# Performance work log

Hardware: AMD Instinct MI355X
Metric: run time of the kernel (lower is better)

The kernel has to match this reference:

```python
import jax, jax.numpy as jnp
import numpy as np

V, K, E, H, B, T = 30000, 9, 300, 300, 64, 512


def _lstm_dir(pre, W_hh, reverse):
    # pre: [T, B, 4H] = x @ W_ih.T + b_ih + b_hh, torch gate order (i, f, g, o)
    Bsz = pre.shape[1]
    Hh = W_hh.shape[1]
    h0 = jnp.zeros((Bsz, Hh), pre.dtype)
    c0 = jnp.zeros((Bsz, Hh), pre.dtype)

    def step(carry, p):
        h, c = carry
        gates = p + h @ W_hh.T
        i, f, g, o = jnp.split(gates, 4, axis=-1)
        i = jax.nn.sigmoid(i)
        f = jax.nn.sigmoid(f)
        o = jax.nn.sigmoid(o)
        g = jnp.tanh(g)
        c = f * c + i * g
        h = o * jnp.tanh(c)
        return (h, c), h

    _, hs = jax.lax.scan(step, (h0, c0), pre, reverse=reverse)
    return hs  # [T, B, H], time-aligned with input (reverse dir handled by scan)


def _crf_loglik(em, tags, mask, start, end, trans):
    # torchcrf CRF log-likelihood, reduction='sum'. em: [B,T,K], mask: [B,T] float.
    em_sc = jnp.take_along_axis(em, tags[..., None], axis=-1)[..., 0]  # [B,T]
    tr_sc = trans[tags[:, :-1], tags[:, 1:]]                            # [B,T-1]
    seq_len = jnp.sum(mask, axis=1).astype(jnp.int32)                   # [B]
    last_tags = jnp.take_along_axis(tags, (seq_len - 1)[:, None], axis=1)[:, 0]
    num = start[tags[:, 0]] + em_sc[:, 0]
    num = num + jnp.sum((tr_sc + em_sc[:, 1:]) * mask[:, 1:], axis=1)
    num = num + end[last_tags]

    # forward algorithm (partition function)
    alpha0 = start[None, :] + em[:, 0]             # [B,K]
    em_t = jnp.swapaxes(em[:, 1:], 0, 1)           # [T-1,B,K]
    m_t = jnp.swapaxes(mask[:, 1:], 0, 1)          # [T-1,B]

    def step(alpha, xs):
        e, m = xs
        nxt = jax.nn.logsumexp(alpha[:, :, None] + trans[None] + e[:, None, :], axis=1)
        return jnp.where(m[:, None] > 0, nxt, alpha), None

    alpha, _ = jax.lax.scan(step, alpha0, (em_t, m_t))
    den = jax.nn.logsumexp(alpha + end[None, :], axis=1)
    return jnp.sum(num - den)


def _forward(x, y, embedding, W_ih_f, W_hh_f, b_ih_f, b_hh_f,
             W_ih_b, W_hh_b, b_ih_b, b_hh_b, W_lin, b_lin,
             start_trans, end_trans, trans):
    emb = embedding[x]                       # [B,T,E]
    emb_t = jnp.swapaxes(emb, 0, 1)          # [T,B,E]
    pre_f = emb_t @ W_ih_f.T + (b_ih_f + b_hh_f)
    pre_b = emb_t @ W_ih_b.T + (b_ih_b + b_hh_b)
    hs_f = _lstm_dir(pre_f, W_hh_f, reverse=False)
    hs_b = _lstm_dir(pre_b, W_hh_b, reverse=True)
    out = jnp.concatenate([hs_f, hs_b], axis=-1)  # [T,B,2H]
    out = jnp.swapaxes(out, 0, 1)                 # [B,T,2H]
    logits = out @ W_lin.T + b_lin
    probs = jax.nn.softmax(logits, axis=-1)
    mask = (y != -1).astype(probs.dtype)
    llh = _crf_loglik(probs, y, mask, start_trans, end_trans, trans)
    return probs, -llh


def setup_inputs() -> dict:
    key = jax.random.key(0)
    ks = jax.random.split(key, 17)

    def p(k, shape, s=0.05):
        return jax.random.normal(k, shape, dtype=jnp.float32) * s

    return {
        "x": jax.random.randint(ks[0], (B, T), 0, V),
        "y": jax.random.randint(ks[1], (B, T), 0, K),
        "embedding": p(ks[2], (V, E), 1.0),
        "W_ih_f": p(ks[3], (4 * H, E)),
        "W_hh_f": p(ks[4], (4 * H, H)),
        "b_ih_f": p(ks[5], (4 * H,)),
        "b_hh_f": p(ks[6], (4 * H,)),
        "W_ih_b": p(ks[7], (4 * H, E)),
        "W_hh_b": p(ks[8], (4 * H, H)),
        "b_ih_b": p(ks[9], (4 * H,)),
        "b_hh_b": p(ks[10], (4 * H,)),
        "W_lin": p(ks[11], (K, 2 * H)),
        "b_lin": p(ks[12], (K,)),
        "start_trans": p(ks[13], (K,), 0.1),
        "end_trans": p(ks[14], (K,), 0.1),
        "trans": p(ks[15], (K, K), 0.1),
    }


def reference(x, y, embedding, W_ih_f, W_hh_f, b_ih_f, b_hh_f,
              W_ih_b, W_hh_b, b_ih_b, b_hh_b, W_lin, b_lin,
              start_trans, end_trans, trans):
    return _forward(x, y, embedding, W_ih_f, W_hh_f, b_ih_f, b_hh_f,
                    W_ih_b, W_hh_b, b_ih_b, b_hh_b, W_lin, b_lin,
                    start_trans, end_trans, trans)
```

## Files before the change

kernel.cpp:

```cpp
#include <hip/hip_runtime.h>
#include <stdint.h>

#define TSEQ 512
#define NB   64
#define EMB  300
#define HID  300
#define G4   1200
#define KKP  150
#define NT   9
#define MTOT (TSEQ*NB)

#define NP 19
#define NQ 4
#define NWG (2*NQ*NP)
#define KSTEPS 10
#define HSTR 164
#define SENT64 0xFFFFFFFFFFFFFFFFull

typedef _Float16 f16x8 __attribute__((ext_vector_type(8)));
typedef float f32x4 __attribute__((ext_vector_type(4)));
union H2U { uint32_t u; _Float16 h[2]; };

__device__ __forceinline__ uint32_t packf2(float a, float b) {
  H2U u; u.h[0] = (_Float16)a; u.h[1] = (_Float16)b; return u.u;
}
__device__ __forceinline__ float fexp(float x) {
  return __builtin_amdgcn_exp2f(x * 1.44269504088896f);
}
__device__ __forceinline__ float sigm(float x) {
  return __builtin_amdgcn_rcpf(1.0f + fexp(-x));
}
__device__ __forceinline__ float ftanh(float x) {
  return 1.0f - 2.0f * __builtin_amdgcn_rcpf(fexp(2.0f * x) + 1.0f);
}

__global__ __launch_bounds__(256) void prep_wih(
    const float* __restrict__ Wihf, const float* __restrict__ Wihb,
    uint32_t* __restrict__ wtih) {
  int i = blockIdx.x * 256 + threadIdx.x;
  if (i >= KKP * G4) return;
  int m = blockIdx.y;
  int kk = i / G4, g = i % G4;
  const float* src = (m == 0) ? Wihf : Wihb;
  float2 v = *(const float2*)(src + (size_t)g * 300 + 2 * kk);
  wtih[(size_t)m * (KKP * G4) + i] = packf2(v.x, v.y);
}

__global__ __launch_bounds__(256) void prep_bias(
    const float* __restrict__ bihf, const float* __restrict__ bhhf,
    const float* __restrict__ bihb, const float* __restrict__ bhhb,
    float* __restrict__ bias) {
  int i = blockIdx.x * 256 + threadIdx.x;
  if (i < G4) {
    bias[i]       = bihf[i] + bhhf[i];
    bias[G4 + i]  = bihb[i] + bhhb[i];
  }
}

__global__ __launch_bounds__(64) void prep_w3(
    const float* __restrict__ Whhf, const float* __restrict__ Whhb,
    uint32_t* __restrict__ w2) {
  int blk = blockIdx.x;
  int ks = blk % KSTEPS; int tmp = blk / KSTEPS;
  int w = tmp & 3; tmp >>= 2;
  int p = tmp % NP; int d = tmp / NP;
  int lane = threadIdx.x;
  const float* W = d ? Whhb : Whhf;
  int m = lane & 15;
  int gamma = m >> 2, rr = m & 3;
  int hid = 16 * p + 4 * w + rr;
  int k0 = ks * 32 + (lane >> 4) * 8;
  float vals[8];
  #pragma unroll
  for (int e = 0; e < 8; ++e) {
    int k = k0 + e;
    vals[e] = (hid < 300 && k < 300) ? W[(size_t)(gamma * 300 + hid) * 300 + k] : 0.0f;
  }
  uint4 dw;
  dw.x = packf2(vals[0], vals[1]);
  dw.y = packf2(vals[2], vals[3]);
  dw.z = packf2(vals[4], vals[5]);
  dw.w = packf2(vals[6], vals[7]);
  *(uint4*)(w2 + ((size_t)blk * 64 + lane) * 4) = dw;
}

__global__ __launch_bounds__(256) void init_sent(uint32_t* __restrict__ ring) {
  size_t i = (size_t)blockIdx.x * 256 + threadIdx.x;
  if (i < 2457600ull)
    ((uint4*)ring)[i] = make_uint4(0xFFFFFFFFu, 0xFFFFFFFFu, 0xFFFFFFFFu, 0xFFFFFFFFu);
}

__global__ __launch_bounds__(256) void gather_emb(
    const int* __restrict__ x, const float* __restrict__ emb,
    uint32_t* __restrict__ Ae) {
  __shared__ __align__(16) uint32_t buf[64 * KKP];
  __shared__ int idxs[64];
  int tid = threadIdx.x;
  int m0 = blockIdx.x * 64;
  if (tid < 64) {
    int mm = m0 + tid;
    idxs[tid] = x[(size_t)(mm & 63) * TSEQ + (mm >> 6)];
  }
  __syncthreads();
  for (int i = tid; i < 64 * KKP; i += 256) {
    int mm = i / KKP, kk = i % KKP;
    float2 v = *(const float2*)(emb + (size_t)idxs[mm] * EMB + 2 * kk);
    buf[i] = packf2(v.x, v.y);
  }
  __syncthreads();
  for (int i = tid; i < 64 * KKP; i += 256) {
    int kk = i >> 6, mm = i & 63;
    Ae[(size_t)kk * MTOT + m0 + mm] = buf[mm * KKP + kk];
  }
}

__global__ __launch_bounds__(256) void embed_pre_mfma(
    const uint32_t* __restrict__ Ae, const uint32_t* __restrict__ wtih,
    const float* __restrict__ bias, _Float16* __restrict__ pre) {
  const int d = blockIdx.z;
  const int tid = threadIdx.x;
  const int w = tid >> 6, lane = tid & 63;
  const int n0 = blockIdx.x * 64 + w * 16;
  const int m00 = blockIdx.y * 128;
  const int col = n0 + (lane & 15);
  const bool colok = col < G4;
  const int rsel = lane >> 4;
  const uint32_t* Wd = wtih + (size_t)d * (KKP * G4);
  uint32_t bfr[KSTEPS][4];
  #pragma unroll
  for (int ks = 0; ks < KSTEPS; ++ks)
    #pragma unroll
    for (int j = 0; j < 4; ++j) {
      int kk = ks * 16 + rsel * 4 + j;
      bfr[ks][j] = (kk < KKP && colok) ? Wd[(size_t)kk * G4 + col] : 0u;
    }
  float bcol = colok ? bias[d * G4 + col] : 0.0f;
  for (int mb = 0; mb < 8; ++mb) {
    const int m0 = m00 + mb * 16;
    uint32_t afr[KSTEPS][4];
    #pragma unroll
    for (int ks = 0; ks < KSTEPS; ++ks)
      #pragma unroll
      for (int j = 0; j < 4; ++j) {
        int kk = ks * 16 + rsel * 4 + j;
        afr[ks][j] = (kk < KKP) ? Ae[(size_t)kk * MTOT + m0 + (lane & 15)] : 0u;
      }
    f32x4 acc; acc[0] = bcol; acc[1] = bcol; acc[2] = bcol; acc[3] = bcol;
    #pragma unroll
    for (int ks = 0; ks < KSTEPS; ++ks) {
      union { uint32_t u[4]; f16x8 v; } au, bu;
      au.u[0] = afr[ks][0]; au.u[1] = afr[ks][1]; au.u[2] = afr[ks][2]; au.u[3] = afr[ks][3];
      bu.u[0] = bfr[ks][0]; bu.u[1] = bfr[ks][1]; bu.u[2] = bfr[ks][2]; bu.u[3] = bfr[ks][3];
      acc = __builtin_amdgcn_mfma_f32_16x16x32_f16(au.v, bu.v, acc, 0, 0, 0);
    }
    if (colok) {
      #pragma unroll
      for (int j = 0; j < 4; ++j) {
        int m = m0 + rsel * 4 + j;
        pre[((size_t)d * MTOT + m) * G4 + col] = (_Float16)acc[j];
      }
    }
  }
}

__global__ __launch_bounds__(256, 1) void lstm_ring(
    const uint32_t* __restrict__ w2, const _Float16* __restrict__ pre,
    uint64_t* __restrict__ ring, uint32_t* __restrict__ hs16) {
  const int wg = blockIdx.x;
  const int p  = wg % NP;
  const int dq = wg / NP;
  const int q  = dq & 3;
  const int d  = dq >> 2;
  const int tid = threadIdx.x;
  const int w = tid >> 6, lane = tid & 63;
  const int G = lane >> 4, b = lane & 15;
  const int hidbase = 16 * p + 4 * w;
  const bool valid = hidbase < 300;
  const int bglob = 16 * q + b;

  __shared__ __align__(16) uint32_t hstg[2][16 * HSTR];
  __shared__ float xch[4][272];

  for (int i = tid; i < 2 * 16 * HSTR; i += 256) ((uint32_t*)hstg)[i] = 0u;

  uint4 afr[KSTEPS];
  const int blk0 = ((d * NP + p) * 4 + w) * KSTEPS;
  #pragma unroll
  for (int ks = 0; ks < KSTEPS; ++ks)
    afr[ks] = *(const uint4*)(w2 + ((size_t)(blk0 + ks) * 64 + lane) * 4);

  const int sb  = tid / 15;
  const int seg = tid % 15;
  const bool stg = tid < 240;

  float cstate = 0.0f;
  __syncthreads();

  for (int s = 0; s < TSEQ; ++s) {
    const int t = d ? (TSEQ - 1 - s) : s;
    const int cur = s & 1;

    uint2 pr = make_uint2(0u, 0u);
    if (valid)
      pr = *(const uint2*)(pre + ((size_t)d * MTOT + (size_t)t * NB + bglob) * G4
                           + (G * 300 + hidbase));

    if (s > 0 && stg) {
      const uint64_t* src = ring + ((size_t)(dq * TSEQ + (s - 1)) * 16 + sb) * 75 + seg * 5;
      uint64_t v[5];
      #pragma unroll
      for (int r = 0; r < 5; ++r)
        v[r] = __hip_atomic_load(src + r, __ATOMIC_RELAXED, __HIP_MEMORY_SCOPE_AGENT);
      uint32_t pend = 0x1Fu;
      while (pend) {
        #pragma unroll
        for (int r = 0; r < 5; ++r) {
          if (pend & (1u << r)) {
            if (v[r] != SENT64) pend &= ~(1u << r);
            else v[r] = __hip_atomic_load(src + r, __ATOMIC_RELAXED,
                                          __HIP_MEMORY_SCOPE_AGENT);
          }
        }
      }
      #pragma unroll
      for (int r = 0; r < 5; ++r)
        *(uint64_t*)&hstg[cur][sb * HSTR + 2 * (seg * 5 + r)] = v[r];
    }
    __syncthreads();

    f32x4 acc0, acc1;
    {
      H2U c0, c1; c0.u = pr.x; c1.u = pr.y;
      acc0[0] = (float)c0.h[0]; acc0[1] = (float)c0.h[1];
      acc0[2] = (float)c1.h[0]; acc0[3] = (float)c1.h[1];
      acc1[0] = 0.f; acc1[1] = 0.f; acc1[2] = 0.f; acc1[3] = 0.f;
    }
    #pragma unroll
    for (int ks = 0; ks < KSTEPS; ks += 2) {
      union { uint4 u; f16x8 v; } au0, au1, bu0, bu1;
      bu0.u = *(const uint4*)&hstg[cur][b * HSTR + ks * 16 + G * 4];
      bu1.u = *(const uint4*)&hstg[cur][b * HSTR + (ks + 1) * 16 + G * 4];
      au0.u = afr[ks]; au1.u = afr[ks + 1];
      acc0 = __builtin_amdgcn_mfma_f32_16x16x32_f16(au0.v, bu0.v, acc0, 0, 0, 0);
      acc1 = __builtin_amdgcn_mfma_f32_16x16x32_f16(au1.v, bu1.v, acc1, 0, 0, 0);
    }

    #pragma unroll
    for (int j = 0; j < 4; ++j)
      xch[w][(j * 4 + G) * 17 + b] = acc0[j] + acc1[j];
    asm volatile("s_waitcnt lgkmcnt(0)" ::: "memory");
    __builtin_amdgcn_sched_barrier(0);
    float gi = xch[w][(G * 4 + 0) * 17 + b];
    float gf = xch[w][(G * 4 + 1) * 17 + b];
    float gg = xch[w][(G * 4 + 2) * 17 + b];
    float go = xch[w][(G * 4 + 3) * 17 + b];

    float iv = sigm(gi), fv = sigm(gf), gv = ftanh(gg), ov = sigm(go);
    float c = fv * cstate + iv * gv; cstate = c;
    float h = ov * ftanh(c);

    float hp = __shfl_xor(h, 16);
    uint32_t dw = packf2(h, hp);
    uint32_t hi = __shfl_xor(dw, 32);
    if (valid && G == 0) {
      uint64_t val = (uint64_t)dw | ((uint64_t)hi << 32);
      __hip_atomic_store(
          ring + ((size_t)(dq * TSEQ + s) * 16 + b) * 75 + (4 * p + w),
          val, __ATOMIC_RELAXED, __HIP_MEMORY_SCOPE_AGENT);
      *(uint64_t*)(hs16 + ((size_t)d * MTOT + (size_t)t * NB + bglob) * 152
                   + (8 * p + 2 * w)) = val;
    }
  }
}

__global__ __launch_bounds__(256) void logits_probs(
    const uint32_t* __restrict__ hs16, const float* __restrict__ Wlin,
    const float* __restrict__ blin, float* __restrict__ probs) {
  __shared__ float Ws[NT * 600];
  __shared__ float bs[NT];
  int tid = threadIdx.x;
  for (int i = tid; i < NT * 600; i += 256) Ws[i] = Wlin[i];
  if (tid < NT) bs[tid] = blin[tid];
  __syncthreads();
  int wave = tid >> 6, lane = tid & 63;
  for (int it = 0; it < 4; ++it) {
    int tb = blockIdx.x * 16 + wave * 4 + it;
    const uint32_t* hf = hs16 + (size_t)tb * 152;
    const uint32_t* hb = hs16 + ((size_t)MTOT + tb) * 152;
    uint32_t fa[3], ga[3];
    fa[0] = hf[lane]; fa[1] = hf[64 + lane];
    fa[2] = (lane < 22) ? hf[128 + lane] : 0u;
    ga[0] = hb[lane]; ga[1] = hb[64 + lane];
    ga[2] = (lane < 22) ? hb[128 + lane] : 0u;
    float p[NT];
    #pragma unroll
    for (int k = 0; k < NT; ++k) p[k] = 0.f;
    #pragma unroll
    for (int c = 0; c < 3; ++c) {
      int kk = c * 64 + lane;
      if (kk < KKP) {
        H2U uf; uf.u = fa[c];
        H2U ug; ug.u = ga[c];
        float hf0 = (float)uf.h[0], hf1 = (float)uf.h[1];
        float hb0 = (float)ug.h[0], hb1 = (float)ug.h[1];
        #pragma unroll
        for (int k = 0; k < NT; ++k)
          p[k] += hf0 * Ws[k * 600 + 2 * kk] + hf1 * Ws[k * 600 + 2 * kk + 1]
                + hb0 * Ws[k * 600 + 300 + 2 * kk] + hb1 * Ws[k * 600 + 300 + 2 * kk + 1];
      }
    }
    #pragma unroll
    for (int off = 32; off > 0; off >>= 1)
      #pragma unroll
      for (int k = 0; k < NT; ++k) p[k] += __shfl_xor(p[k], off);
    float l[NT]; float mx = -1e30f;
    #pragma unroll
    for (int k = 0; k < NT; ++k) { l[k] = p[k] + bs[k]; mx = fmaxf(mx, l[k]); }
    float ssum = 0.f;
    #pragma unroll
    for (int k = 0; k < NT; ++k) ssum += expf(l[k] - mx);
    int t = tb >> 6, bb = tb & 63;
    if (lane < NT)
      probs[((size_t)bb * TSEQ + t) * NT + lane] = expf(l[lane] - mx) / ssum;
  }
}

__global__ __launch_bounds__(256) void crf_num(
    const int* __restrict__ y, const float* __restrict__ probs,
    const float* __restrict__ strt, const float* __restrict__ endt,
    const float* __restrict__ trans, float* __restrict__ nums) {
  int b = blockIdx.x, tid = threadIdx.x;
  __shared__ float r1[256], r2[256];
  float s = 0.f, cnt = 0.f;
  for (int t = tid; t < TSEQ; t += 256) {
    int yc = y[(size_t)b * TSEQ + t];
    cnt += (yc != -1) ? 1.f : 0.f;
    if (t >= 1) {
      int yp = y[(size_t)b * TSEQ + t - 1];
      float mask = (yc != -1) ? 1.f : 0.f;
      s += mask * (trans[yp * NT + yc] + probs[((size_t)b * TSEQ + t) * NT + yc]);
    }
  }
  r1[tid] = s; r2[tid] = cnt;
  __syncthreads();
  for (int off = 128; off > 0; off >>= 1) {
    if (tid < off) { r1[tid] += r1[tid + off]; r2[tid] += r2[tid + off]; }
    __syncthreads();
  }
  if (tid == 0) {
    int y0 = y[(size_t)b * TSEQ];
    int seqlen = (int)(r2[0] + 0.5f);
    int ylast = y[(size_t)b * TSEQ + seqlen - 1];
    nums[b] = strt[y0] + probs[((size_t)b * TSEQ) * NT + y0] + r1[0] + endt[ylast];
  }
}

__global__ __launch_bounds__(64) void crf_alpha(
    const int* __restrict__ y, const float* __restrict__ probs,
    const float* __restrict__ strt, const float* __restrict__ endt,
    const float* __restrict__ trans, float* __restrict__ dens) {
  int b = blockIdx.x, lane = threadIdx.x;
  __shared__ float P[TSEQ * NT];
  __shared__ float msk[TSEQ];
  for (int i = lane; i < TSEQ * NT; i += 64) P[i] = probs[(size_t)b * TSEQ * NT + i];
  for (int i = lane; i < TSEQ; i += 64) msk[i] = (y[(size_t)b * TSEQ + i] != -1) ? 1.f : 0.f;
  asm volatile("s_waitcnt lgkmcnt(0) vmcnt(0)" ::: "memory");
  int li = lane < NT ? lane : NT - 1;
  float trc[NT];
  #pragma unroll
  for (int j = 0; j < NT; ++j) trc[j] = trans[j * NT + li];
  float al = strt[li] + P[li];
  for (int t = 1; t < TSEQ; ++t) {
    float e = P[t * NT + li];
    float m = msk[t];
    float tmp[NT]; float mx = -1e30f;
    #pragma unroll
    for (int j = 0; j < NT; ++j) {
      float aj = __shfl(al, j);
      tmp[j] = aj + trc[j];
      mx = fmaxf(mx, tmp[j]);
    }
    float sum = 0.f;
    #pragma unroll
    for (int j = 0; j < NT; ++j) sum += expf(tmp[j] - mx);
    float nxt = e + mx + logf(sum);
    al = (m > 0.5f) ? nxt : al;
  }
  float vv = al + endt[li];
  float mx = -1e30f;
  #pragma unroll
  for (int j = 0; j < NT; ++j) mx = fmaxf(mx, __shfl(vv, j));
  float sum = 0.f;
  #pragma unroll
  for (int j = 0; j < NT; ++j) sum += expf(__shfl(vv, j) - mx);
  if (lane == 0) dens[b] = mx + logf(sum);
}

__global__ __launch_bounds__(64) void final_sum(
    const float* __restrict__ nums, const float* __restrict__ dens,
    float* __restrict__ out) {
  __shared__ float r[64];
  int tid = threadIdx.x;
  r[tid] = nums[tid] - dens[tid];
  __syncthreads();
  for (int off = 32; off > 0; off >>= 1) {
    if (tid < off) r[tid] += r[tid + off];
    __syncthreads();
  }
  if (tid == 0) out[(size_t)MTOT * NT] = -r[0];
}

extern "C" void kernel_launch(void* const* d_in, const int* in_sizes, int n_in,
                              void* d_out, int out_size, void* d_ws, size_t ws_size,
                              hipStream_t stream) {
  (void)in_sizes; (void)n_in; (void)out_size;
  const int*   x     = (const int*)d_in[0];
  const int*   y     = (const int*)d_in[1];
  const float* emb   = (const float*)d_in[2];
  const float* Wihf  = (const float*)d_in[3];
  const float* Whhf  = (const float*)d_in[4];
  const float* bihf  = (const float*)d_in[5];
  const float* bhhf  = (const float*)d_in[6];
  const float* Wihb  = (const float*)d_in[7];
  const float* Whhb  = (const float*)d_in[8];
  const float* bihb  = (const float*)d_in[9];
  const float* bhhb  = (const float*)d_in[10];
  const float* Wlin  = (const float*)d_in[11];
  const float* blin  = (const float*)d_in[12];
  const float* strt  = (const float*)d_in[13];
  const float* endt  = (const float*)d_in[14];
  const float* trans = (const float*)d_in[15];
  float* outp = (float*)d_out;

  char* ws = (char*)d_ws;
  const size_t OFF_WTIH = 0;
  const size_t OFF_W2   = 1440000;
  const size_t OFF_BIAS = 2996480;
  const size_t OFF_NUMS = 3006080;
  const size_t OFF_DENS = 3006336;
  const size_t OFF_RING = 3006592;
  const size_t OFF_HS16 = 42328192;
  const size_t OFF_PRE  = 82174080;
  if (ws_size < 239460480ull) return;

  uint32_t* wtih = (uint32_t*)(ws + OFF_WTIH);
  uint32_t* w2   = (uint32_t*)(ws + OFF_W2);
  float*    bias = (float*)(ws + OFF_BIAS);
  float*    nums = (float*)(ws + OFF_NUMS);
  float*    dens = (float*)(ws + OFF_DENS);
  uint32_t* ring = (uint32_t*)(ws + OFF_RING);
  uint32_t* Ae   = (uint32_t*)(ws + OFF_RING);
  uint32_t* hs16 = (uint32_t*)(ws + OFF_HS16);
  _Float16* pre  = (_Float16*)(ws + OFF_PRE);

  prep_wih<<<dim3((KKP * G4 + 255) / 256, 2), 256, 0, stream>>>(Wihf, Wihb, wtih);
  prep_bias<<<dim3((G4 + 255) / 256), 256, 0, stream>>>(bihf, bhhf, bihb, bhhb, bias);
  prep_w3<<<dim3(2 * NP * 4 * KSTEPS), 64, 0, stream>>>(Whhf, Whhb, w2);
  gather_emb<<<dim3(MTOT / 64), 256, 0, stream>>>(x, emb, Ae);
  embed_pre_mfma<<<dim3(19, MTOT / 128, 2), 256, 0, stream>>>(Ae, wtih, bias, pre);
  init_sent<<<dim3((2457600 + 255) / 256), 256, 0, stream>>>(ring);
  lstm_ring<<<dim3(NWG), 256, 0, stream>>>(w2, pre, (uint64_t*)ring, hs16);
  logits_probs<<<dim3(MTOT / 16), 256, 0, stream>>>(hs16, Wlin, blin, outp);
  crf_num<<<dim3(NB), 256, 0, stream>>>(y, outp, strt, endt, trans, nums);
  crf_alpha<<<dim3(NB), 64, 0, stream>>>(y, outp, strt, endt, trans, dens);
  final_sum<<<1, 64, 0, stream>>>(nums, dens, outp);
}
```

Before: 2.108 ms.

## Use sc0 inline-asm ring loads with bounded spin and hs16 fallback polling

Replaces the per-slot atomic polling of the cross-workgroup h ring with a batched inline-asm poll of five dwordx2 loads using the sc0 cache bit. The poll gives up after a fixed spin count and falls back to waiting on the hs16 output buffer, which is now also sentinel-initialised and written atomically. Sentinel detection moves to per-32-bit halves, and the workgroup-to-(p,dq) mapping is interleaved so that producer and consumer groups are spread differently across CUs. This aims to cut the recurrent handoff latency on each step, at the cost of extra sentinel init traffic and a coherence dependence on the sc0 cache behaviour.

```diff
diff --git a/kernel.cpp b/kernel.cpp
--- a/kernel.cpp
+++ b/kernel.cpp
@@ -15,7 +15,8 @@
 #define NWG (2*NQ*NP)
 #define KSTEPS 10
 #define HSTR 164
-#define SENT64 0xFFFFFFFFFFFFFFFFull
+#define SENT32 0xFFFFFFFFu
+#define MAXSPIN 16
 
 typedef _Float16 f16x8 __attribute__((ext_vector_type(8)));
 typedef float f32x4 __attribute__((ext_vector_type(4)));
@@ -32,6 +33,15 @@
 }
 __device__ __forceinline__ float ftanh(float x) {
   return 1.0f - 2.0f * __builtin_amdgcn_rcpf(fexp(2.0f * x) + 1.0f);
+}
+__device__ __forceinline__ bool valid64(uint64_t v) {
+  return ((uint32_t)v != SENT32) & ((uint32_t)(v >> 32) != SENT32);
+}
+__device__ __forceinline__ uint64_t fb_wait(uint64_t cur, const uint64_t* p) {
+  uint64_t x = cur;
+  while (!valid64(x))
+    x = __hip_atomic_load(p, __ATOMIC_RELAXED, __HIP_MEMORY_SCOPE_AGENT);
+  return x;
 }
 
 __global__ __launch_bounds__(256) void prep_wih(
@@ -84,10 +94,12 @@
   *(uint4*)(w2 + ((size_t)blk * 64 + lane) * 4) = dw;
 }
 
-__global__ __launch_bounds__(256) void init_sent(uint32_t* __restrict__ ring) {
+__global__ __launch_bounds__(256) void init_sent(
+    uint32_t* __restrict__ ring, uint32_t* __restrict__ hs16) {
   size_t i = (size_t)blockIdx.x * 256 + threadIdx.x;
-  if (i < 2457600ull)
-    ((uint4*)ring)[i] = make_uint4(0xFFFFFFFFu, 0xFFFFFFFFu, 0xFFFFFFFFu, 0xFFFFFFFFu);
+  uint4 f = make_uint4(SENT32, SENT32, SENT32, SENT32);
+  if (i < 2457600ull) ((uint4*)ring)[i] = f;
+  if (i < 2490368ull) ((uint4*)hs16)[i] = f;
 }
 
 __global__ __launch_bounds__(256) void gather_emb(
@@ -167,8 +179,8 @@
     const uint32_t* __restrict__ w2, const _Float16* __restrict__ pre,
     uint64_t* __restrict__ ring, uint32_t* __restrict__ hs16) {
   const int wg = blockIdx.x;
-  const int p  = wg % NP;
-  const int dq = wg / NP;
+  const int dq = wg & 7;
+  const int p  = wg >> 3;
   const int q  = dq & 3;
   const int d  = dq >> 2;
   const int tid = threadIdx.x;
@@ -206,25 +218,40 @@
                            + (G * 300 + hidbase));
 
     if (s > 0 && stg) {
-      const uint64_t* src = ring + ((size_t)(dq * TSEQ + (s - 1)) * 16 + sb) * 75 + seg * 5;
-      uint64_t v[5];
-      #pragma unroll
-      for (int r = 0; r < 5; ++r)
-        v[r] = __hip_atomic_load(src + r, __ATOMIC_RELAXED, __HIP_MEMORY_SCOPE_AGENT);
-      uint32_t pend = 0x1Fu;
-      while (pend) {
-        #pragma unroll
-        for (int r = 0; r < 5; ++r) {
-          if (pend & (1u << r)) {
-            if (v[r] != SENT64) pend &= ~(1u << r);
-            else v[r] = __hip_atomic_load(src + r, __ATOMIC_RELAXED,
-                                          __HIP_MEMORY_SCOPE_AGENT);
-          }
-        }
+      const uint64_t* srcL = ring + ((size_t)(dq * TSEQ + (s - 1)) * 16 + sb) * 75
+                             + seg * 5;
+      uint64_t v0, v1, v2, v3, v4;
+      int spins = 0;
+      bool done = false;
+      do {
+        asm volatile(
+            "global_load_dwordx2 %0, %5, off sc0\n\t"
+            "global_load_dwordx2 %1, %5, off offset:8 sc0\n\t"
+            "global_load_dwordx2 %2, %5, off offset:16 sc0\n\t"
+            "global_load_dwordx2 %3, %5, off offset:24 sc0\n\t"
+            "global_load_dwordx2 %4, %5, off offset:32 sc0\n\t"
+            "s_waitcnt vmcnt(0)"
+            : "=v"(v0), "=v"(v1), "=v"(v2), "=v"(v3), "=v"(v4)
+            : "v"(srcL)
+            : "memory");
+        done = valid64(v0) & valid64(v1) & valid64(v2) & valid64(v3) & valid64(v4);
+      } while (!done && ++spins < MAXSPIN);
+      if (!done) {
+        const int tprev = d ? (TSEQ - 1 - (s - 1)) : (s - 1);
+        const uint64_t* fb = (const uint64_t*)(hs16 +
+            ((size_t)d * MTOT + (size_t)tprev * NB + 16 * q + sb) * 152) + seg * 5;
+        v0 = fb_wait(v0, fb + 0);
+        v1 = fb_wait(v1, fb + 1);
+        v2 = fb_wait(v2, fb + 2);
+        v3 = fb_wait(v3, fb + 3);
+        v4 = fb_wait(v4, fb + 4);
       }
-      #pragma unroll
-      for (int r = 0; r < 5; ++r)
-        *(uint64_t*)&hstg[cur][sb * HSTR + 2 * (seg * 5 + r)] = v[r];
+      uint32_t* dstL = &hstg[cur][sb * HSTR + 2 * (seg * 5)];
+      *(uint64_t*)(dstL + 0) = v0;
+      *(uint64_t*)(dstL + 2) = v1;
+      *(uint64_t*)(dstL + 4) = v2;
+      *(uint64_t*)(dstL + 6) = v3;
+      *(uint64_t*)(dstL + 8) = v4;
     }
     __syncthreads();
 
@@ -264,11 +291,13 @@
     uint32_t hi = __shfl_xor(dw, 32);
     if (valid && G == 0) {
       uint64_t val = (uint64_t)dw | ((uint64_t)hi << 32);
+      const int slot = 4 * p + w;
+      uint64_t* dstL = ring + ((size_t)(dq * TSEQ + s) * 16 + b) * 75 + slot;
+      asm volatile("global_store_dwordx2 %0, %1, off sc0"
+                   :: "v"(dstL), "v"(val) : "memory");
       __hip_atomic_store(
-          ring + ((size_t)(dq * TSEQ + s) * 16 + b) * 75 + (4 * p + w),
+          (uint64_t*)(hs16 + ((size_t)d * MTOT + (size_t)t * NB + bglob) * 152) + slot,
           val, __ATOMIC_RELAXED, __HIP_MEMORY_SCOPE_AGENT);
-      *(uint64_t*)(hs16 + ((size_t)d * MTOT + (size_t)t * NB + bglob) * 152
-                   + (8 * p + 2 * w)) = val;
     }
   }
 }
@@ -458,7 +487,7 @@
   prep_w3<<<dim3(2 * NP * 4 * KSTEPS), 64, 0, stream>>>(Whhf, Whhb, w2);
   gather_emb<<<dim3(MTOT / 64), 256, 0, stream>>>(x, emb, Ae);
   embed_pre_mfma<<<dim3(19, MTOT / 128, 2), 256, 0, stream>>>(Ae, wtih, bias, pre);
-  init_sent<<<dim3((2457600 + 255) / 256), 256, 0, stream>>>(ring);
+  init_sent<<<dim3((2490368 + 255) / 256), 256, 0, stream>>>(ring, hs16);
   lstm_ring<<<dim3(NWG), 256, 0, stream>>>(w2, pre, (uint64_t*)ring, hs16);
   logits_probs<<<dim3(MTOT / 16), 256, 0, stream>>>(hs16, Wlin, blin, outp);
   crf_num<<<dim3(NB), 256, 0, stream>>>(y, outp, strt, endt, trans, nums);
```

Result: slower. 2.870 ms (+36.2%).
